# Performance work log

Hardware: AMD Instinct MI355X
Metric: run time of the kernel (lower is better)

The kernel has to match this reference:

```python
import jax, jax.numpy as jnp
import numpy as np

BS, L, IMG, RS = 512, 68, 224, 7
R2 = RS * RS
DEPTH_SCALE = 500.0
VALID_RANGE = 90.0
THR = 1e-4


def setup_inputs() -> dict:
    key = jax.random.key(0)
    k1, k2, k3 = jax.random.split(key, 3)
    rel_depth_pred = jax.random.normal(k1, (BS, L, L), dtype=jnp.float32)
    depth = jax.random.uniform(k2, (BS, 1, IMG, IMG), dtype=jnp.float32)
    # landmarks in pixel coords well inside the 224px image so regions are valid
    landmarks = jax.random.uniform(k3, (BS, L, 2), dtype=jnp.float32) * 180.0 + 22.0
    scale_factor = jnp.ones((BS, 2), dtype=jnp.float32)
    bbox = jnp.zeros((BS, 4), dtype=jnp.float32)
    return {"rel_depth_pred": rel_depth_pred, "depth": depth,
            "landmarks": landmarks, "scale_factor": scale_factor, "bbox": bbox}


def _extract_landmark_depth(depth, landmarks, scale_factor, bbox):
    bs, img = depth.shape[0], depth.shape[3]
    # normalized landmark coords in [-1, 1]
    face_lm = (landmarks - bbox[:, None, :2]) * scale_factor[:, None, :] / img * 2.0 - 1.0  # [bs,L,2]
    x = jnp.linspace(-RS / 2.0, RS / 2.0, RS) / img * 2.0
    A, B = jnp.meshgrid(x, x, indexing='ij')          # A[i,j]=x[i], B[i,j]=x[j]
    offsets = jnp.stack([B, A], axis=2)               # torch: stack(meshgrid([x,x])[::-1], dim=2)
    grid = face_lm[:, :, None, None, :] + offsets     # [bs,L,RS,RS,2]
    grid = grid.reshape(bs, L * R2, 2)
    # F.grid_sample mode='nearest', padding='zeros', align_corners=False
    ix = ((grid[..., 0] + 1.0) * img - 1.0) * 0.5
    iy = ((grid[..., 1] + 1.0) * img - 1.0) * 0.5
    xi = jnp.round(ix).astype(jnp.int32)
    yi = jnp.round(iy).astype(jnp.int32)
    valid = (xi >= 0) & (xi < img) & (yi >= 0) & (yi < img)
    xi = jnp.clip(xi, 0, img - 1)
    yi = jnp.clip(yi, 0, img - 1)
    flat = depth.reshape(bs, img * img)
    vals = jnp.take_along_axis(flat, yi * img + xi, axis=1) * valid.astype(depth.dtype)
    regions = vals.reshape(bs, L, R2)
    s = jnp.sort(regions, axis=2)                     # ascending per landmark region
    m = s > THR
    m = m.at[:, :, 0].set(False)                      # torch zeroes index 0 before the diff
    trans = m[:, :, 1:] & ~m[:, :, :-1]               # single 0->1 transition (m is monotone)
    has = jnp.any(trans, axis=2)
    st = jnp.where(has, jnp.argmax(trans, axis=2) + 1, R2 - 1)  # fallback: last index
    med_ind = (st + R2 - 1) // 2                      # ((st + 48)/2).long()
    median = jnp.take_along_axis(s, med_ind[..., None], axis=2)[..., 0]  # [bs,L]
    # torch.median over dim=1: lower median = (L-1)//2-th order statistic
    med_of_med = jnp.sort(median, axis=1)[:, (L - 1) // 2]
    median_mask = jnp.abs(median - med_of_med[:, None]) < VALID_RANGE / DEPTH_SCALE
    return median, median_mask


def reference(rel_depth_pred, depth, landmarks, scale_factor, bbox):
    median, median_mask = _extract_landmark_depth(depth, landmarks, scale_factor, bbox)
    median = median * DEPTH_SCALE
    median_diff = median[:, :, None] - median[:, None, :]            # [bs,L,L]
    fm = median_mask.astype(rel_depth_pred.dtype)
    median_rel_mask = fm[:, :, None] * fm[:, None, :]                # [bs,L,L]
    d = rel_depth_pred - median_diff
    ad = jnp.abs(d)
    loss_ele = jnp.where(ad < 1.0, 0.5 * d * d, ad - 0.5)            # smooth_l1, reduction='none'
    loss = jnp.sum(loss_ele * median_rel_mask) / (jnp.sum(median_rel_mask) + 1e-4)
    return loss, median_diff, median_rel_mask
```

## Files before the change

kernel.cpp:

```cpp
#include <hip/hip_runtime.h>
#include <cfloat>
#include <math.h>

static constexpr int kBS  = 512;
static constexpr int kL   = 68;
static constexpr int kIMG = 224;
static constexpr int kR2  = 49;
static constexpr int kLL  = kL * kL;
static constexpr int kChunks = 5;
static constexpr int kOutBlocks = kBS * kChunks;

__device__ __forceinline__ float lin_off(int k) {
  float step = __fdiv_rn((float)k, 6.0f);
  float a = __fmul_rn(-3.5f, __fsub_rn(1.0f, step));
  float b = __fmul_rn(3.5f, step);
  float x = __fadd_rn(a, b);
  return __fmul_rn(__fdiv_rn(x, 224.0f), 2.0f);
}

__global__ __launch_bounds__(256) void k_median(
    const float* __restrict__ depth, const float* __restrict__ lmk,
    const float* __restrict__ scale, const float* __restrict__ bbox,
    float* __restrict__ med) {
  int wave = blockIdx.x * 4 + (threadIdx.x >> 6);
  int lane = threadIdx.x & 63;
  if (wave >= kBS * kL) return;
  int b = wave / kL;

  float lmx = lmk[wave * 2 + 0];
  float lmy = lmk[wave * 2 + 1];
  float sx = scale[b * 2 + 0], sy = scale[b * 2 + 1];
  float bx = bbox[b * 4 + 0],  by = bbox[b * 4 + 1];

  float tx = __fsub_rn(lmx, bx);
  tx = __fmul_rn(tx, sx); tx = __fdiv_rn(tx, 224.0f); tx = __fmul_rn(tx, 2.0f);
  float flmx = __fsub_rn(tx, 1.0f);
  float ty = __fsub_rn(lmy, by);
  ty = __fmul_rn(ty, sy); ty = __fdiv_rn(ty, 224.0f); ty = __fmul_rn(ty, 2.0f);
  float flmy = __fsub_rn(ty, 1.0f);

  float v = INFINITY;
  if (lane < kR2) {
    int i = lane / 7, j = lane - i * 7;
    float gx = __fadd_rn(flmx, lin_off(j));
    float gy = __fadd_rn(flmy, lin_off(i));
    float ix = __fmul_rn(__fsub_rn(__fmul_rn(__fadd_rn(gx, 1.0f), 224.0f), 1.0f), 0.5f);
    float iy = __fmul_rn(__fsub_rn(__fmul_rn(__fadd_rn(gy, 1.0f), 224.0f), 1.0f), 0.5f);
    int xi = (int)rintf(ix), yi = (int)rintf(iy);
    bool valid = (xi >= 0) && (xi < kIMG) && (yi >= 0) && (yi < kIMG);
    int xc = min(max(xi, 0), kIMG - 1), yc = min(max(yi, 0), kIMG - 1);
    float dv = depth[(size_t)b * (kIMG * kIMG) + yc * kIMG + xc];
    v = valid ? dv : 0.0f;
  }

  unsigned long long mle = __ballot(lane < kR2 && v <= 1e-4f);
  int cnt = __popcll(mle);

#pragma unroll
  for (int k = 2; k <= 64; k <<= 1) {
#pragma unroll
    for (int j = k >> 1; j > 0; j >>= 1) {
      float w = __shfl_xor(v, j, 64);
      bool up = ((lane & k) == 0);
      bool lower = ((lane & j) == 0);
      v = (up == lower) ? fminf(v, w) : fmaxf(v, w);
    }
  }

  int st = min(max(cnt, 1), kR2 - 1);
  int kk = (st + kR2 - 1) >> 1;
  float m = __shfl(v, kk, 64);
  if (lane == 0) med[wave] = m;
}

__global__ __launch_bounds__(256) void k_out(
    const float* __restrict__ rdp, const float* __restrict__ med,
    float* __restrict__ out_diff, float* __restrict__ out_mask,
    double* __restrict__ part) {
  __shared__ float s_med[kL], s_m[kL], s_f[kL];
  __shared__ float mom_s;
  __shared__ double sn[4], sd[4];
  int b = blockIdx.y, chunk = blockIdx.x, t = threadIdx.x;

  if (t < kL) s_med[t] = med[b * kL + t];
  __syncthreads();
  if (t < kL) {
    float v = s_med[t];
    int rank = 0;
    for (int j = 0; j < kL; ++j) {
      float vj = s_med[j];
      rank += ((vj < v) || (vj == v && j < t)) ? 1 : 0;
    }
    if (rank == (kL - 1) / 2) mom_s = v;
  }
  __syncthreads();
  if (t < kL) {
    float v = s_med[t];
    s_m[t] = __fmul_rn(v, 500.0f);
    s_f[t] = (fabsf(__fsub_rn(v, mom_s)) < 0.18f) ? 1.0f : 0.0f;
  }
  __syncthreads();

  int e = chunk * 1024 + t * 4;
  double pn = 0.0, pd = 0.0;
  if (e < kLL) {
    unsigned i = (unsigned)e / (unsigned)kL;
    int j = e - (int)i * kL;
    size_t base = (size_t)b * kLL + e;
    float4 rp = *(const float4*)(rdp + base);
    float mi = s_m[i], fi = s_f[i];
    float rq[4] = {rp.x, rp.y, rp.z, rp.w};
#pragma unroll
    for (int q = 0; q < 4; ++q) {
      float mj = s_m[j + q], fj = s_f[j + q];
      float diff = __fsub_rn(mi, mj);
      float mv = __fmul_rn(fi, fj);
      out_diff[base + q] = diff;
      out_mask[base + q] = mv;
      float d = __fsub_rn(rq[q], diff);
      float ad = fabsf(d);
      float le = (ad < 1.0f) ? __fmul_rn(__fmul_rn(0.5f, d), d)
                             : __fsub_rn(ad, 0.5f);
      pn += (double)__fmul_rn(le, mv);
      pd += (double)mv;
    }
  }

  for (int off = 32; off > 0; off >>= 1) {
    pn += __shfl_down(pn, off, 64);
    pd += __shfl_down(pd, off, 64);
  }
  int w = t >> 6;
  if ((t & 63) == 0) { sn[w] = pn; sd[w] = pd; }
  __syncthreads();
  if (t == 0) {
    int blkid = b * kChunks + chunk;
    part[2 * blkid + 0] = sn[0] + sn[1] + sn[2] + sn[3];
    part[2 * blkid + 1] = sd[0] + sd[1] + sd[2] + sd[3];
  }
}

__global__ __launch_bounds__(256) void k_final(
    const double* __restrict__ part, float* __restrict__ out0) {
  __shared__ double sn[4], sd[4];
  double pn = 0.0, pd = 0.0;
  for (int i = threadIdx.x; i < kOutBlocks; i += 256) {
    pn += part[2 * i + 0];
    pd += part[2 * i + 1];
  }
  for (int off = 32; off > 0; off >>= 1) {
    pn += __shfl_down(pn, off, 64);
    pd += __shfl_down(pd, off, 64);
  }
  int w = threadIdx.x >> 6;
  if ((threadIdx.x & 63) == 0) { sn[w] = pn; sd[w] = pd; }
  __syncthreads();
  if (threadIdx.x == 0) {
    double tn = sn[0] + sn[1] + sn[2] + sn[3];
    double td = sd[0] + sd[1] + sd[2] + sd[3];
    out0[0] = (float)(tn / (td + 1e-4));
  }
}

extern "C" void kernel_launch(void* const* d_in, const int* in_sizes, int n_in,
                              void* d_out, int out_size, void* d_ws, size_t ws_size,
                              hipStream_t stream) {
  const float* rdp   = (const float*)d_in[0];
  const float* depth = (const float*)d_in[1];
  const float* lmk   = (const float*)d_in[2];
  const float* scale = (const float*)d_in[3];
  const float* bbox  = (const float*)d_in[4];

  float* out = (float*)d_out;
  float* out_diff = out + 1;
  float* out_mask = out + 1 + (size_t)kBS * kLL;

  char* ws = (char*)d_ws;
  float*  med  = (float*)(ws);
  double* part = (double*)(ws + 139264);

  int nWaves = kBS * kL;
  int nBlk1 = (nWaves + 3) / 4;
  k_median<<<dim3(nBlk1), dim3(256), 0, stream>>>(depth, lmk, scale, bbox, med);
  k_out<<<dim3(kChunks, kBS), dim3(256), 0, stream>>>(rdp, med, out_diff, out_mask, part);
  k_final<<<dim3(1), dim3(256), 0, stream>>>(part, out);
}
```

Before: 171.5 us.

## Fuse median extraction and loss output into one per-batch kernel

Merges the per-landmark median kernel and the output/loss kernel into a single kernel with one 1024-thread block per batch element. Sixteen waves loop over the 68 landmarks and write their medians straight to shared memory, which removes the global round trip for medians and one kernel launch. The output loop now covers the whole 68x68 matrix per block and writes diff and mask with float4 stores. In exchange, each block runs its gather-and-sort phase serially over about five landmarks per wave, which lowers parallelism in that phase. The float4 stores land on output pointers offset by one float, so they are only 4-byte aligned.

Result: no change. 172.5 us (+0.6%).

```diff
diff --git a/kernel.cpp b/kernel.cpp
--- a/kernel.cpp
+++ b/kernel.cpp
@@ -1,5 +1,4 @@
 #include <hip/hip_runtime.h>
-#include <cfloat>
 #include <math.h>
 
 static constexpr int kBS  = 512;
@@ -7,8 +6,7 @@
 static constexpr int kIMG = 224;
 static constexpr int kR2  = 49;
 static constexpr int kLL  = kL * kL;
-static constexpr int kChunks = 5;
-static constexpr int kOutBlocks = kBS * kChunks;
+static constexpr int kG4  = kLL / 4;
 
 __device__ __forceinline__ float lin_off(int k) {
   float step = __fdiv_rn((float)k, 6.0f);
@@ -18,72 +16,74 @@
   return __fmul_rn(__fdiv_rn(x, 224.0f), 2.0f);
 }
 
-__global__ __launch_bounds__(256) void k_median(
+__global__ __launch_bounds__(1024) void k_fused(
     const float* __restrict__ depth, const float* __restrict__ lmk,
     const float* __restrict__ scale, const float* __restrict__ bbox,
-    float* __restrict__ med) {
-  int wave = blockIdx.x * 4 + (threadIdx.x >> 6);
-  int lane = threadIdx.x & 63;
-  if (wave >= kBS * kL) return;
-  int b = wave / kL;
-
-  float lmx = lmk[wave * 2 + 0];
-  float lmy = lmk[wave * 2 + 1];
-  float sx = scale[b * 2 + 0], sy = scale[b * 2 + 1];
-  float bx = bbox[b * 4 + 0],  by = bbox[b * 4 + 1];
-
-  float tx = __fsub_rn(lmx, bx);
-  tx = __fmul_rn(tx, sx); tx = __fdiv_rn(tx, 224.0f); tx = __fmul_rn(tx, 2.0f);
-  float flmx = __fsub_rn(tx, 1.0f);
-  float ty = __fsub_rn(lmy, by);
-  ty = __fmul_rn(ty, sy); ty = __fdiv_rn(ty, 224.0f); ty = __fmul_rn(ty, 2.0f);
-  float flmy = __fsub_rn(ty, 1.0f);
-
-  float v = INFINITY;
-  if (lane < kR2) {
-    int i = lane / 7, j = lane - i * 7;
-    float gx = __fadd_rn(flmx, lin_off(j));
-    float gy = __fadd_rn(flmy, lin_off(i));
-    float ix = __fmul_rn(__fsub_rn(__fmul_rn(__fadd_rn(gx, 1.0f), 224.0f), 1.0f), 0.5f);
-    float iy = __fmul_rn(__fsub_rn(__fmul_rn(__fadd_rn(gy, 1.0f), 224.0f), 1.0f), 0.5f);
-    int xi = (int)rintf(ix), yi = (int)rintf(iy);
-    bool valid = (xi >= 0) && (xi < kIMG) && (yi >= 0) && (yi < kIMG);
-    int xc = min(max(xi, 0), kIMG - 1), yc = min(max(yi, 0), kIMG - 1);
-    float dv = depth[(size_t)b * (kIMG * kIMG) + yc * kIMG + xc];
-    v = valid ? dv : 0.0f;
-  }
-
-  unsigned long long mle = __ballot(lane < kR2 && v <= 1e-4f);
-  int cnt = __popcll(mle);
-
-#pragma unroll
-  for (int k = 2; k <= 64; k <<= 1) {
-#pragma unroll
-    for (int j = k >> 1; j > 0; j >>= 1) {
-      float w = __shfl_xor(v, j, 64);
-      bool up = ((lane & k) == 0);
-      bool lower = ((lane & j) == 0);
-      v = (up == lower) ? fminf(v, w) : fmaxf(v, w);
-    }
-  }
-
-  int st = min(max(cnt, 1), kR2 - 1);
-  int kk = (st + kR2 - 1) >> 1;
-  float m = __shfl(v, kk, 64);
-  if (lane == 0) med[wave] = m;
-}
-
-__global__ __launch_bounds__(256) void k_out(
-    const float* __restrict__ rdp, const float* __restrict__ med,
+    const float* __restrict__ rdp,
     float* __restrict__ out_diff, float* __restrict__ out_mask,
     double* __restrict__ part) {
   __shared__ float s_med[kL], s_m[kL], s_f[kL];
   __shared__ float mom_s;
-  __shared__ double sn[4], sd[4];
-  int b = blockIdx.y, chunk = blockIdx.x, t = threadIdx.x;
+  __shared__ double sn[16], sd[16];
 
-  if (t < kL) s_med[t] = med[b * kL + t];
+  const int b = blockIdx.x;
+  const int t = threadIdx.x;
+  const int w = t >> 6, lane = t & 63;
+
+  const float sx = scale[b * 2 + 0], sy = scale[b * 2 + 1];
+  const float bx = bbox[b * 4 + 0],  by = bbox[b * 4 + 1];
+
+  float loff = lin_off(lane < 7 ? lane : 0);
+  int si = 0, sj = 0;
+  if (lane < kR2) { si = lane / 7; sj = lane - si * 7; }
+  const float offx = __shfl(loff, sj, 64);
+  const float offy = __shfl(loff, si, 64);
+  const size_t dbase = (size_t)b * (kIMG * kIMG);
+
+  for (int l = w; l < kL; l += 16) {
+    float lmx = lmk[(b * kL + l) * 2 + 0];
+    float lmy = lmk[(b * kL + l) * 2 + 1];
+    float tx = __fsub_rn(lmx, bx);
+    tx = __fmul_rn(tx, sx); tx = __fdiv_rn(tx, 224.0f); tx = __fmul_rn(tx, 2.0f);
+    float flmx = __fsub_rn(tx, 1.0f);
+    float ty = __fsub_rn(lmy, by);
+    ty = __fmul_rn(ty, sy); ty = __fdiv_rn(ty, 224.0f); ty = __fmul_rn(ty, 2.0f);
+    float flmy = __fsub_rn(ty, 1.0f);
+
+    float v = INFINITY;
+    if (lane < kR2) {
+      float gx = __fadd_rn(flmx, offx);
+      float gy = __fadd_rn(flmy, offy);
+      float ix = __fmul_rn(__fsub_rn(__fmul_rn(__fadd_rn(gx, 1.0f), 224.0f), 1.0f), 0.5f);
+      float iy = __fmul_rn(__fsub_rn(__fmul_rn(__fadd_rn(gy, 1.0f), 224.0f), 1.0f), 0.5f);
+      int xi = (int)rintf(ix), yi = (int)rintf(iy);
+      bool valid = (xi >= 0) && (xi < kIMG) && (yi >= 0) && (yi < kIMG);
+      int xc = min(max(xi, 0), kIMG - 1), yc = min(max(yi, 0), kIMG - 1);
+      float dv = depth[dbase + yc * kIMG + xc];
+      v = valid ? dv : 0.0f;
+    }
+
+    unsigned long long mle = __ballot(lane < kR2 && v <= 1e-4f);
+    int cnt = __popcll(mle);
+
+#pragma unroll
+    for (int k = 2; k <= 64; k <<= 1) {
+#pragma unroll
+      for (int j = k >> 1; j > 0; j >>= 1) {
+        float ww = __shfl_xor(v, j, 64);
+        bool up = ((lane & k) == 0);
+        bool lower = ((lane & j) == 0);
+        v = (up == lower) ? fminf(v, ww) : fmaxf(v, ww);
+      }
+    }
+
+    int st = min(max(cnt, 1), kR2 - 1);
+    int kk = (st + kR2 - 1) >> 1;
+    float m = __shfl(v, kk, 64);
+    if (lane == 0) s_med[l] = m;
+  }
   __syncthreads();
+
   if (t < kL) {
     float v = s_med[t];
     int rank = 0;
@@ -101,22 +101,23 @@
   }
   __syncthreads();
 
-  int e = chunk * 1024 + t * 4;
   double pn = 0.0, pd = 0.0;
-  if (e < kLL) {
-    unsigned i = (unsigned)e / (unsigned)kL;
-    int j = e - (int)i * kL;
+  for (int g = t; g < kG4; g += 1024) {
+    int e = g * 4;
+    unsigned iu = (unsigned)e / (unsigned)kL;
+    int i = (int)iu;
+    int j = e - i * kL;
     size_t base = (size_t)b * kLL + e;
     float4 rp = *(const float4*)(rdp + base);
     float mi = s_m[i], fi = s_f[i];
     float rq[4] = {rp.x, rp.y, rp.z, rp.w};
+    float df[4], mk[4];
 #pragma unroll
     for (int q = 0; q < 4; ++q) {
       float mj = s_m[j + q], fj = s_f[j + q];
       float diff = __fsub_rn(mi, mj);
       float mv = __fmul_rn(fi, fj);
-      out_diff[base + q] = diff;
-      out_mask[base + q] = mv;
+      df[q] = diff; mk[q] = mv;
       float d = __fsub_rn(rq[q], diff);
       float ad = fabsf(d);
       float le = (ad < 1.0f) ? __fmul_rn(__fmul_rn(0.5f, d), d)
@@ -124,19 +125,22 @@
       pn += (double)__fmul_rn(le, mv);
       pd += (double)mv;
     }
+    *(float4*)(out_diff + base) = make_float4(df[0], df[1], df[2], df[3]);
+    *(float4*)(out_mask + base) = make_float4(mk[0], mk[1], mk[2], mk[3]);
   }
 
   for (int off = 32; off > 0; off >>= 1) {
     pn += __shfl_down(pn, off, 64);
     pd += __shfl_down(pd, off, 64);
   }
-  int w = t >> 6;
-  if ((t & 63) == 0) { sn[w] = pn; sd[w] = pd; }
+  if (lane == 0) { sn[w] = pn; sd[w] = pd; }
   __syncthreads();
   if (t == 0) {
-    int blkid = b * kChunks + chunk;
-    part[2 * blkid + 0] = sn[0] + sn[1] + sn[2] + sn[3];
-    part[2 * blkid + 1] = sd[0] + sd[1] + sd[2] + sd[3];
+    double tn = 0.0, td = 0.0;
+#pragma unroll
+    for (int k = 0; k < 16; ++k) { tn += sn[k]; td += sd[k]; }
+    part[2 * b + 0] = tn;
+    part[2 * b + 1] = td;
   }
 }
 
@@ -144,7 +148,7 @@
     const double* __restrict__ part, float* __restrict__ out0) {
   __shared__ double sn[4], sd[4];
   double pn = 0.0, pd = 0.0;
-  for (int i = threadIdx.x; i < kOutBlocks; i += 256) {
+  for (int i = threadIdx.x; i < kBS; i += 256) {
     pn += part[2 * i + 0];
     pd += part[2 * i + 1];
   }
@@ -175,13 +179,9 @@
   float* out_diff = out + 1;
   float* out_mask = out + 1 + (size_t)kBS * kLL;
 
-  char* ws = (char*)d_ws;
-  float*  med  = (float*)(ws);
-  double* part = (double*)(ws + 139264);
+  double* part = (double*)d_ws;
 
-  int nWaves = kBS * kL;
-  int nBlk1 = (nWaves + 3) / 4;
-  k_median<<<dim3(nBlk1), dim3(256), 0, stream>>>(depth, lmk, scale, bbox, med);
-  k_out<<<dim3(kChunks, kBS), dim3(256), 0, stream>>>(rdp, med, out_diff, out_mask, part);
+  k_fused<<<dim3(kBS), dim3(1024), 0, stream>>>(depth, lmk, scale, bbox, rdp,
+                                                out_diff, out_mask, part);
   k_final<<<dim3(1), dim3(256), 0, stream>>>(part, out);
 }
```
